# Kernel optimization log

Measured on AMD Instinct MI355X. Metric: run time of the kernel, lower is better.

Reference implementation:

```python
import jax, jax.numpy as jnp
import numpy as np

B = 1024          # batch
H = 512           # hidden_dim
T = 256           # seq_len
CD = 2            # coord_dim
LAT = 64 + 64 + 128  # total latent dim


def setup_inputs() -> dict:
    key = jax.random.key(0)
    ks = jax.random.split(key, 20)
    s = 0.05  # weight init scale
    rn = lambda k, shp: (jax.random.normal(k, shp, dtype=jnp.float32) * s)
    return {
        "z_primitive": jax.random.normal(ks[0], (B, 64), dtype=jnp.float32),
        "z_skill": jax.random.normal(ks[1], (B, 64), dtype=jnp.float32),
        "z_style": jax.random.normal(ks[2], (B, 128), dtype=jnp.float32),
        "W_proj": rn(ks[3], (2 * H, LAT)),
        "b_proj": jnp.zeros((2 * H,), jnp.float32),
        "Wih1": rn(ks[4], (4 * H, CD)),
        "Whh1": rn(ks[5], (4 * H, H)),
        "bih1": jnp.zeros((4 * H,), jnp.float32),
        "bhh1": jnp.zeros((4 * H,), jnp.float32),
        "Wih2": rn(ks[6], (4 * H, H)),
        "Whh2": rn(ks[7], (4 * H, H)),
        "bih2": jnp.zeros((4 * H,), jnp.float32),
        "bhh2": jnp.zeros((4 * H,), jnp.float32),
        "Wo1": rn(ks[8], (H // 2, H)),
        "bo1": jnp.zeros((H // 2,), jnp.float32),
        "Wo2": rn(ks[9], (CD, H // 2)),
        "bo2": jnp.zeros((CD,), jnp.float32),
    }


def _lstm_cell(x, h, c, Wih, Whh, bih, bhh):
    # PyTorch gate order: i, f, g, o
    gates = x @ Wih.T + h @ Whh.T + (bih + bhh)
    i, f, g, o = jnp.split(gates, 4, axis=1)
    c_new = jax.nn.sigmoid(f) * c + jax.nn.sigmoid(i) * jnp.tanh(g)
    h_new = jax.nn.sigmoid(o) * jnp.tanh(c_new)
    return h_new, c_new


def reference(z_primitive, z_skill, z_style, W_proj, b_proj,
              Wih1, Whh1, bih1, bhh1, Wih2, Whh2, bih2, bhh2,
              Wo1, bo1, Wo2, bo2):
    z = jnp.concatenate([z_primitive, z_skill, z_style], axis=1)  # [B, LAT]
    init = z @ W_proj.T + b_proj                                  # [B, 2H]
    h0 = init[:, :H]
    c0 = init[:, H:]
    x0 = jnp.zeros((z.shape[0], CD), init.dtype)

    def step(carry, _):
        x, h1, c1, h2, c2 = carry
        h1, c1 = _lstm_cell(x, h1, c1, Wih1, Whh1, bih1, bhh1)
        h2, c2 = _lstm_cell(h1, h2, c2, Wih2, Whh2, bih2, bhh2)
        # output MLP (Dropout inactive in eval)
        y = jax.nn.relu(h2 @ Wo1.T + bo1) @ Wo2.T + bo2  # [B, CD]
        return (y, h1, c1, h2, c2), y

    # h0/c0 repeated across both LSTM layers (repeat(2,1,1) in torch)
    _, ys = jax.lax.scan(step, (x0, h0, c0, h0, c0), None, length=T)
    return jnp.transpose(ys, (1, 0, 2))  # [B, T, CD]
```

## Files before the change

kernel.cpp:

```cpp
#include <hip/hip_runtime.h>
#include <math.h>

#define NB 1024
#define NH 512
#define NT 256
#define NCD 2

typedef unsigned short u16;
typedef __bf16 bf16x8 __attribute__((ext_vector_type(8)));
typedef float  f32x4  __attribute__((ext_vector_type(4)));
typedef unsigned int  u32x4 __attribute__((ext_vector_type(4)));

#define MFMA_BF16 __builtin_amdgcn_mfma_f32_16x16x32_bf16

__device__ __forceinline__ float sigf(float x) { return 1.0f / (1.0f + expf(-x)); }
__device__ __forceinline__ u16 f2b(float f) {
    union { float f; unsigned i; } v; v.f = f;
    unsigned r = v.i + 0x7fffu + ((v.i >> 16) & 1u);
    return (u16)(r >> 16);
}

__device__ __forceinline__ void async_cp16(const void* gptr, void* lptr) {
    __builtin_amdgcn_global_load_lds(
        (const __attribute__((address_space(1))) unsigned int*)gptr,
        (__attribute__((address_space(3))) unsigned int*)lptr,
        16, 0, 0);
}

__device__ __forceinline__ u32x4 aload16(const u16* p) {
    unsigned* q = (unsigned*)(void*)p;
    u32x4 v;
    v.x = __hip_atomic_load(q + 0, __ATOMIC_RELAXED, __HIP_MEMORY_SCOPE_AGENT);
    v.y = __hip_atomic_load(q + 1, __ATOMIC_RELAXED, __HIP_MEMORY_SCOPE_AGENT);
    v.z = __hip_atomic_load(q + 2, __ATOMIC_RELAXED, __HIP_MEMORY_SCOPE_AGENT);
    v.w = __hip_atomic_load(q + 3, __ATOMIC_RELAXED, __HIP_MEMORY_SCOPE_AGENT);
    return v;
}

__global__ __launch_bounds__(256) void convert3(
    const float* __restrict__ a, const float* __restrict__ b,
    const float* __restrict__ c,
    u16* __restrict__ oa, u16* __restrict__ ob, u16* __restrict__ oc)
{
    const int i = blockIdx.x * 256 + threadIdx.x;
    oa[i] = f2b(a[i]); ob[i] = f2b(b[i]); oc[i] = f2b(c[i]);
}

__global__ __launch_bounds__(256) void convw1(
    const float* __restrict__ a, u16* __restrict__ o)
{
    const int i = blockIdx.x * 256 + threadIdx.x;
    o[i] = f2b(a[i]);
}

__global__ __launch_bounds__(256) void bsum_k(
    const float* __restrict__ bi1, const float* __restrict__ bh1,
    const float* __restrict__ bi2, const float* __restrict__ bh2,
    float* __restrict__ o1, float* __restrict__ o2)
{
    const int i = blockIdx.x * 256 + threadIdx.x;
    o1[i] = bi1[i] + bh1[i];
    o2[i] = bi2[i] + bh2[i];
}

__global__ __launch_bounds__(512) void zero_bar(unsigned* __restrict__ b)
{
    b[threadIdx.x] = 0u;
}

__global__ __launch_bounds__(256) void init_kernel(
    const float* __restrict__ zp, const float* __restrict__ zs,
    const float* __restrict__ zst, const float* __restrict__ Wp,
    const float* __restrict__ bp,
    u16* __restrict__ h1, float* __restrict__ c1,
    u16* __restrict__ h2, float* __restrict__ c2)
{
    __shared__ float z[4][256];
    const int tid = threadIdx.x;
    const int b0  = blockIdx.x * 4;
    for (int i = tid; i < 4 * 256; i += 256) {
        const int bb = i >> 8, k = i & 255;
        float v;
        if (k < 64)       v = zp [(b0 + bb) * 64  + k];
        else if (k < 128) v = zs [(b0 + bb) * 64  + (k - 64)];
        else              v = zst[(b0 + bb) * 128 + (k - 128)];
        z[bb][k] = v;
    }
    __syncthreads();
    for (int rt = 0; rt < 4; ++rt) {
        const int r = rt * 256 + tid;
        const float bias = bp[r];
        float a0 = bias, a1 = bias, a2 = bias, a3 = bias;
        for (int k = 0; k < 256; ++k) {
            const float w = Wp[r * 256 + k];
            a0 += z[0][k] * w; a1 += z[1][k] * w;
            a2 += z[2][k] * w; a3 += z[3][k] * w;
        }
        const float acc[4] = {a0, a1, a2, a3};
        for (int bb = 0; bb < 4; ++bb) {
            const int b = b0 + bb;
            if (r < NH) {
                h1[b * NH + r] = f2b(acc[bb]);
                h2[b * NH + r] = f2b(acc[bb]);
            } else {
                c1[b * NH + r - NH] = acc[bb];
                c2[b * NH + r - NH] = acc[bb];
            }
        }
    }
}

__global__ __launch_bounds__(512, 4) void step_fused(
    const u16* __restrict__ h2prev,
    const u16* __restrict__ A0,
    const u16* __restrict__ W0,
    const float* __restrict__ bsum1,
    const float* __restrict__ Wx,
    const u16* __restrict__ W1b,
    const float* __restrict__ bo1, const float* __restrict__ Wo2,
    const float* __restrict__ bo2, float* __restrict__ outp,
    float* __restrict__ c1, u16* __restrict__ h1next,
    const u16* __restrict__ Wih2b, const u16* __restrict__ Whh2b,
    const float* __restrict__ bsum2,
    float* __restrict__ c2, const u16* __restrict__ h2cur,
    u16* __restrict__ h2next,
    unsigned* bar,
    const int t, const int do_lstm)
{
    __shared__ __align__(16) char smem[61440];
    float* eg  = (float*)smem;
    float* red = (float*)(smem + 36864);

    const int tid  = threadIdx.x;
    const int lane = tid & 63;
    const int wv   = tid >> 6;
    const int g    = wv & 3;
    const int mh   = wv >> 2;
    const int l15  = lane & 15;
    const int q    = lane >> 4;
    const int bx   = blockIdx.x;
    const int ut   = (bx & 7) * 2 + ((bx >> 3) & 1);
    const int grp  = bx >> 4;
    const int b0   = grp * 32;
    const int u0   = ut * 32;

    int goffW0, goffW1, goffA = 0, goffO[4];
    {
        const int c0 = (wv * 2) * 64 + lane;
        const int w0r = c0 >> 3;
        goffW0 = ((w0r >> 5) * NH + u0 + (w0r & 31)) * NH + (((c0 & 7) ^ (w0r & 7)) * 8);
        const int c1i = (wv * 2 + 1) * 64 + lane;
        const int w1r = c1i >> 3;
        goffW1 = ((w1r >> 5) * NH + u0 + (w1r & 31)) * NH + (((c1i & 7) ^ (w1r & 7)) * 8);
        if (wv < 4) {
            const int ca = wv * 64 + lane;
            const int ar = ca >> 3;
            goffA = (b0 + ar) * NH + (((ca & 7) ^ (ar & 7)) * 8);
        }
#pragma unroll
        for (int i = 0; i < 4; ++i) {
            const int cidx = (wv * 4 + i) * 64 + lane;
            const int row  = cidx >> 3;
            const int kc   = (cidx & 7) ^ (row & 7);
            goffO[i] = row * NH + kc * 8;
        }
    }

    auto issue = [&](int m, int bi) {
        const int k0 = (m & 7) * 64;
        char* base = smem + bi * 20480;
        async_cp16((const void*)(W0 + goffW0 + k0),
                   (void*)(base + 4096 + (wv * 2) * 1024));
        async_cp16((const void*)(W0 + goffW1 + k0),
                   (void*)(base + 4096 + (wv * 2 + 1) * 1024));
        if (wv < 4)
            async_cp16((const void*)(A0 + goffA + k0),
                       (void*)(base + wv * 1024));
    };
    auto issueW2 = [&](const u16* Wp, int m, int bi) {
        const int k0 = (m & 7) * 64;
        char* base = smem + bi * 20480;
        async_cp16((const void*)(Wp + goffW0 + k0), (void*)(base + 4096 + (wv * 2) * 1024));
        async_cp16((const void*)(Wp + goffW1 + k0), (void*)(base + 4096 + (wv * 2 + 1) * 1024));
    };
    auto awrite = [&](char* base, u32x4 v) {
        *(u32x4*)(base + wv * 1024 + lane * 16) = v;
    };

    const int u_e  = tid & 31;
    const int bq_e = tid >> 5;
    const int ug_e = u0 + u_e;
    float bs1r[4], bs2r[4], wx0[4], wx1[4], c1pre[2], c2pre[2];
#pragma unroll
    for (int g4 = 0; g4 < 4; ++g4) {
        bs1r[g4] = bsum1[g4 * NH + ug_e];
        bs2r[g4] = bsum2[g4 * NH + ug_e];
        wx0[g4]  = Wx[(g4 * NH + ug_e) * 2 + 0];
        wx1[g4]  = Wx[(g4 * NH + ug_e) * 2 + 1];
    }
    c1pre[0] = c1[(size_t)(b0 + bq_e * 2 + 0) * NH + ug_e];
    c1pre[1] = c1[(size_t)(b0 + bq_e * 2 + 1) * NH + ug_e];
    c2pre[0] = c2[(size_t)(b0 + bq_e * 2 + 0) * NH + ug_e];
    c2pre[1] = c2[(size_t)(b0 + bq_e * 2 + 1) * NH + ug_e];

    if (do_lstm) issue(0, 2);

    float r_x[4] = {0.f, 0.f, 0.f, 0.f};

    if (h2prev) {
        f32x4 acc_o[2][2];
#pragma unroll
        for (int mi = 0; mi < 2; ++mi)
#pragma unroll
            for (int ni = 0; ni < 2; ++ni)
                acc_o[mi][ni] = (f32x4){0.f, 0.f, 0.f, 0.f};

        for (int kk = 0; kk < 8; ++kk) {
            __syncthreads();
            const int k0 = kk * 64;
#pragma unroll
            for (int i = 0; i < 4; ++i)
                async_cp16((const void*)(W1b + goffO[i] + k0),
                           (void*)(smem + ((wv * 4 + i) << 10)));
            if (wv < 4)
                async_cp16((const void*)(h2prev + goffA + k0),
                           (void*)(smem + 32768 + (wv << 10)));
            asm volatile("s_waitcnt vmcnt(0)" ::: "memory");
            __builtin_amdgcn_s_barrier();
#pragma unroll
            for (int kh = 0; kh < 2; ++kh) {
                bf16x8 bfr[2], av[2];
#pragma unroll
                for (int ni = 0; ni < 2; ++ni) {
                    const int wrow = wv * 32 + ni * 16 + l15;
                    const int j = (kh * 4 + q) ^ (wrow & 7);
                    bfr[ni] = *(const bf16x8*)(smem + wrow * 128 + j * 16);
                }
#pragma unroll
                for (int mi = 0; mi < 2; ++mi) {
                    const int row = mi * 16 + l15;
                    const int j = (kh * 4 + q) ^ (row & 7);
                    av[mi] = *(const bf16x8*)(smem + 32768 + row * 128 + j * 16);
                }
#pragma unroll
                for (int mi = 0; mi < 2; ++mi)
#pragma unroll
                    for (int ni = 0; ni < 2; ++ni)
                        acc_o[mi][ni] = MFMA_BF16(av[mi], bfr[ni], acc_o[mi][ni], 0, 0, 0);
            }
        }
        float bo1n[2], w20[2], w21[2];
#pragma unroll
        for (int ni = 0; ni < 2; ++ni) {
            const int n = wv * 32 + ni * 16 + l15;
            bo1n[ni] = bo1[n]; w20[ni] = Wo2[n]; w21[ni] = Wo2[256 + n];
        }
        float pa[2][4], pb[2][4];
#pragma unroll
        for (int mi = 0; mi < 2; ++mi)
#pragma unroll
            for (int r = 0; r < 4; ++r) {
                const float s0 = fmaxf(acc_o[mi][0][r] + bo1n[0], 0.f);
                const float s1 = fmaxf(acc_o[mi][1][r] + bo1n[1], 0.f);
                pa[mi][r] = s0 * w20[0] + s1 * w20[1];
                pb[mi][r] = s0 * w21[0] + s1 * w21[1];
            }
#pragma unroll
        for (int off = 1; off < 16; off <<= 1)
#pragma unroll
            for (int mi = 0; mi < 2; ++mi)
#pragma unroll
                for (int r = 0; r < 4; ++r) {
                    pa[mi][r] += __shfl_xor(pa[mi][r], off, 64);
                    pb[mi][r] += __shfl_xor(pb[mi][r], off, 64);
                }
        if (l15 == 0) {
#pragma unroll
            for (int mi = 0; mi < 2; ++mi)
#pragma unroll
                for (int r = 0; r < 4; ++r) {
                    const int m = mi * 16 + q * 4 + r;
                    red[m * 16 + wv * 2 + 0] = pa[mi][r];
                    red[m * 16 + wv * 2 + 1] = pb[mi][r];
                }
        }
        __syncthreads();
        if (ut == 0 && tid < 64) {
            const int bl = tid >> 1, cc = tid & 1;
            float y = bo2[cc];
#pragma unroll
            for (int w8 = 0; w8 < 8; ++w8) y += red[bl * 16 + w8 * 2 + cc];
            outp[(size_t)(b0 + bl) * (NT * NCD) + (t - 1) * NCD + cc] = y;
        }
        if (do_lstm) {
#pragma unroll
            for (int jj = 0; jj < 2; ++jj)
#pragma unroll
                for (int cc = 0; cc < 2; ++cc) {
                    float y = bo2[cc];
#pragma unroll
                    for (int w8 = 0; w8 < 8; ++w8)
                        y += red[(bq_e * 2 + jj) * 16 + w8 * 2 + cc];
                    r_x[jj * 2 + cc] = y;
                }
        }
        __syncthreads();
    }
    if (!do_lstm) return;

    {
        f32x4 acc[2];
        acc[0] = (f32x4){0.f, 0.f, 0.f, 0.f};
        acc[1] = (f32x4){0.f, 0.f, 0.f, 0.f};
        const int M = 8;
        issue(1, 0);
        int ci = 2;
        for (int m = 0; m < M; ++m) {
            if (m + 1 < M) {
                if (wv < 4) asm volatile("s_waitcnt vmcnt(3)" ::: "memory");
                else        asm volatile("s_waitcnt vmcnt(2)" ::: "memory");
            } else {
                asm volatile("s_waitcnt vmcnt(0)" ::: "memory");
            }
            __builtin_amdgcn_s_barrier();
            if (m + 2 < M) {
                int bi = ci + 2; if (bi >= 3) bi -= 3;
                issue(m + 2, bi);
            }
            const char* bA = smem + ci * 20480;
            const char* bW = bA + 4096;
#pragma unroll
            for (int khi = 0; khi < 2; ++khi) {
                bf16x8 bfr[2];
#pragma unroll
                for (int ni = 0; ni < 2; ++ni) {
                    const int wrow = g * 32 + ni * 16 + l15;
                    const int j = (khi * 4 + q) ^ (wrow & 7);
                    bfr[ni] = *(const bf16x8*)(bW + wrow * 128 + j * 16);
                }
                const int row = mh * 16 + l15;
                const int j = (khi * 4 + q) ^ (row & 7);
                const bf16x8 av = *(const bf16x8*)(bA + row * 128 + j * 16);
                acc[0] = MFMA_BF16(av, bfr[0], acc[0], 0, 0, 0);
                acc[1] = MFMA_BF16(av, bfr[1], acc[1], 0, 0, 0);
            }
            ++ci; if (ci == 3) ci = 0;
        }

        __syncthreads();
#pragma unroll
        for (int ni = 0; ni < 2; ++ni)
#pragma unroll
            for (int r = 0; r < 4; ++r)
                eg[(g * 32 + mh * 16 + q * 4 + r) * 33 + ni * 16 + l15] = acc[ni][r];
        __syncthreads();

#pragma unroll
        for (int jj = 0; jj < 2; ++jj) {
            const int bl = bq_e * 2 + jj;
            const int b  = b0 + bl;
            float gv[4];
#pragma unroll
            for (int g4 = 0; g4 < 4; ++g4) gv[g4] = eg[(g4 * 32 + bl) * 33 + u_e] + bs1r[g4];
            const float x0 = r_x[jj * 2 + 0];
            const float x1 = r_x[jj * 2 + 1];
#pragma unroll
            for (int g4 = 0; g4 < 4; ++g4) gv[g4] += x0 * wx0[g4] + x1 * wx1[g4];
            const float iv = sigf(gv[0]);
            const float fv = sigf(gv[1]);
            const float gg = tanhf(gv[2]);
            const float ov = sigf(gv[3]);
            const size_t idx = (size_t)b * NH + ug_e;
            const float cn = fv * c1pre[jj] + iv * gg;
            c1[idx] = cn;
            const unsigned hb = (unsigned)f2b(ov * tanhf(cn));
            const unsigned pr = (unsigned)__shfl_xor((int)hb, 1, 64);
            if (!(u_e & 1))
                __hip_atomic_store((unsigned*)(void*)(h1next + idx),
                                   hb | (pr << 16),
                                   __ATOMIC_RELAXED, __HIP_MEMORY_SCOPE_AGENT);
        }
    }

    {
        unsigned* mybar = bar + grp * 16;
        const unsigned target = 16u * (unsigned)(t + 1);
        __syncthreads();
        if (tid == 0) {
            __hip_atomic_fetch_add(mybar, 1u, __ATOMIC_RELAXED, __HIP_MEMORY_SCOPE_AGENT);
            int guard = 0;
            while (__hip_atomic_load(mybar, __ATOMIC_RELAXED, __HIP_MEMORY_SCOPE_AGENT)
                       < target && ++guard < (1 << 20)) {
                __builtin_amdgcn_s_sleep(1);
            }
        }
        __syncthreads();
    }

    {
        f32x4 acc[2];
        acc[0] = (f32x4){0.f, 0.f, 0.f, 0.f};
        acc[1] = (f32x4){0.f, 0.f, 0.f, 0.f};
        u32x4 rB0, rB1;
        if (wv < 4) rB0 = aload16(h1next + goffA);
        issueW2(Wih2b, 0, 0);
        if (wv < 4) rB1 = aload16(h1next + goffA + 64);
        issueW2(Wih2b, 1, 1);
        if (wv < 4) {
            awrite(smem + 0 * 20480, rB0);
            awrite(smem + 1 * 20480, rB1);
            rB0 = aload16(h1next + goffA + 128);
        }
        int ci = 0;
        for (int m = 0; m < 16; ++m) {
            if (m + 1 < 16) {
                if (wv < 4) asm volatile("s_waitcnt vmcnt(6) lgkmcnt(0)" ::: "memory");
                else        asm volatile("s_waitcnt vmcnt(2)" ::: "memory");
            } else {
                asm volatile("s_waitcnt vmcnt(0) lgkmcnt(0)" ::: "memory");
            }
            __builtin_amdgcn_s_barrier();
            if (m + 2 < 16) {
                int bi = ci + 2; if (bi >= 3) bi -= 3;
                if (wv < 4) awrite(smem + bi * 20480, (m & 1) ? rB1 : rB0);
                issueW2((m + 2 < 8) ? Wih2b : Whh2b, m + 2, bi);
                if (wv < 4 && m + 3 < 16) {
                    const u16* Ap = (m + 3 < 8) ? h1next : h2cur;
                    const int k0 = ((m + 3) & 7) * 64;
                    if (m & 1) rB0 = aload16(Ap + goffA + k0);
                    else       rB1 = aload16(Ap + goffA + k0);
                }
            }
            const char* bA = smem + ci * 20480;
            const char* bW = bA + 4096;
#pragma unroll
            for (int khi = 0; khi < 2; ++khi) {
                bf16x8 bfr[2];
#pragma unroll
                for (int ni = 0; ni < 2; ++ni) {
                    const int wrow = g * 32 + ni * 16 + l15;
                    const int j = (khi * 4 + q) ^ (wrow & 7);
                    bfr[ni] = *(const bf16x8*)(bW + wrow * 128 + j * 16);
                }
                const int row = mh * 16 + l15;
                const int j = (khi * 4 + q) ^ (row & 7);
                const bf16x8 av = *(const bf16x8*)(bA + row * 128 + j * 16);
                acc[0] = MFMA_BF16(av, bfr[0], acc[0], 0, 0, 0);
                acc[1] = MFMA_BF16(av, bfr[1], acc[1], 0, 0, 0);
            }
            ++ci; if (ci == 3) ci = 0;
        }

        __syncthreads();
#pragma unroll
        for (int ni = 0; ni < 2; ++ni)
#pragma unroll
            for (int r = 0; r < 4; ++r)
                eg[(g * 32 + mh * 16 + q * 4 + r) * 33 + ni * 16 + l15] = acc[ni][r];
        __syncthreads();

#pragma unroll
        for (int jj = 0; jj < 2; ++jj) {
            const int bl = bq_e * 2 + jj;
            const int b  = b0 + bl;
            float gv[4];
#pragma unroll
            for (int g4 = 0; g4 < 4; ++g4) gv[g4] = eg[(g4 * 32 + bl) * 33 + u_e] + bs2r[g4];
            const float iv = sigf(gv[0]);
            const float fv = sigf(gv[1]);
            const float gg = tanhf(gv[2]);
            const float ov = sigf(gv[3]);
            const size_t idx = (size_t)b * NH + ug_e;
            const float cn = fv * c2pre[jj] + iv * gg;
            c2[idx] = cn;
            h2next[idx] = f2b(ov * tanhf(cn));
        }
    }
}

extern "C" void kernel_launch(void* const* d_in, const int* in_sizes, int n_in,
                              void* d_out, int out_size, void* d_ws, size_t ws_size,
                              hipStream_t stream)
{
    const float* zp   = (const float*)d_in[0];
    const float* zsk  = (const float*)d_in[1];
    const float* zst  = (const float*)d_in[2];
    const float* Wp   = (const float*)d_in[3];
    const float* bp   = (const float*)d_in[4];
    const float* Wih1 = (const float*)d_in[5];
    const float* Whh1 = (const float*)d_in[6];
    const float* bih1 = (const float*)d_in[7];
    const float* bhh1 = (const float*)d_in[8];
    const float* Wih2 = (const float*)d_in[9];
    const float* Whh2 = (const float*)d_in[10];
    const float* bih2 = (const float*)d_in[11];
    const float* bhh2 = (const float*)d_in[12];
    const float* Wo1  = (const float*)d_in[13];
    const float* bo1  = (const float*)d_in[14];
    const float* Wo2  = (const float*)d_in[15];
    const float* bo2  = (const float*)d_in[16];

    const size_t BH = (size_t)NB * NH;
    u16*   h1a   = (u16*)d_ws;
    u16*   h1b   = h1a + BH;
    u16*   h2a   = h1b + BH;
    u16*   h2b   = h2a + BH;
    float* c1    = (float*)(h2b + BH);
    float* c2    = c1 + BH;
    float* bs1   = c2 + BH;
    float* bs2   = bs1 + 2048;
    u16*   Wo1b  = (u16*)(bs2 + 2048);
    u16*   Whh1b = Wo1b + 131072;
    u16*   Wih2b = Whh1b + 1048576;
    u16*   Whh2b = Wih2b + 1048576;
    unsigned* bar = (unsigned*)(Whh2b + 1048576);

    convert3<<<(2048 * 512) / 256, 256, 0, stream>>>(Whh1, Wih2, Whh2, Whh1b, Wih2b, Whh2b);
    convw1<<<(256 * 512) / 256, 256, 0, stream>>>(Wo1, Wo1b);
    bsum_k<<<2048 / 256, 256, 0, stream>>>(bih1, bhh1, bih2, bhh2, bs1, bs2);
    init_kernel<<<NB / 4, 256, 0, stream>>>(zp, zsk, zst, Wp, bp, h1a, c1, h2a, c2);
    zero_bar<<<1, 512, 0, stream>>>(bar);

    u16* h1c = h1a; u16* h1n = h1b;
    u16* h2c = h2a; u16* h2n = h2b;
    float* outp = (float*)d_out;
    for (int t = 0; t < NT; ++t) {
        step_fused<<<512, 512, 0, stream>>>(
            (t == 0) ? (const u16*)0 : h2c, h1c, Whh1b, bs1, Wih1,
            Wo1b, bo1, Wo2, bo2, outp, c1, h1n,
            Wih2b, Whh2b, bs2, c2, h2c, h2n, bar, t, 1);
        u16* tmp = h1c; h1c = h1n; h1n = tmp;
        tmp = h2c; h2c = h2n; h2n = tmp;
    }
    step_fused<<<512, 512, 0, stream>>>(
        h2c, h1c, Whh1b, bs1, Wih1,
        Wo1b, bo1, Wo2, bo2, outp, c1, h1n,
        Wih2b, Whh2b, bs2, c2, h2c, h2n, bar, NT, 0);
}
```

Before: 8.335 ms.

## Split output MLP across blocks with atomic reduction and reorder layer-2 GEMM to overlap barrier

Each block now computes only its 16-column slice of the output MLP, with a triple-buffered async-copy pipeline. Partial results are accumulated into the output with atomicAdd, so the output is zeroed beforehand. A per-group barrier makes all blocks' partial sums visible before the next input x is read back. Layer 2 now runs the h2·Whh2 half first and waits on a second barrier for h1next only partway through, overlapping that barrier with useful MFMA work. The cost is extra atomics and grid-level barrier traffic, and correctness depends on relaxed-atomic visibility and the barrier counter layout.

```diff
diff --git a/kernel.cpp b/kernel.cpp
--- a/kernel.cpp
+++ b/kernel.cpp
@@ -25,6 +25,10 @@
         (const __attribute__((address_space(1))) unsigned int*)gptr,
         (__attribute__((address_space(3))) unsigned int*)lptr,
         16, 0, 0);
+}
+
+__device__ __forceinline__ float aloadf(const float* p) {
+    return __hip_atomic_load((float*)p, __ATOMIC_RELAXED, __HIP_MEMORY_SCOPE_AGENT);
 }
 
 __device__ __forceinline__ u32x4 aload16(const u16* p) {
@@ -66,6 +70,11 @@
 __global__ __launch_bounds__(512) void zero_bar(unsigned* __restrict__ b)
 {
     b[threadIdx.x] = 0u;
+}
+
+__global__ __launch_bounds__(512) void zero_out(float* __restrict__ o)
+{
+    o[blockIdx.x * 512 + threadIdx.x] = 0.f;
 }
 
 __global__ __launch_bounds__(256) void init_kernel(
@@ -111,7 +120,7 @@
 }
 
 __global__ __launch_bounds__(512, 4) void step_fused(
-    const u16* __restrict__ h2prev,
+    const u16* __restrict__ h2c,
     const u16* __restrict__ A0,
     const u16* __restrict__ W0,
     const float* __restrict__ bsum1,
@@ -122,14 +131,12 @@
     float* __restrict__ c1, u16* __restrict__ h1next,
     const u16* __restrict__ Wih2b, const u16* __restrict__ Whh2b,
     const float* __restrict__ bsum2,
-    float* __restrict__ c2, const u16* __restrict__ h2cur,
-    u16* __restrict__ h2next,
-    unsigned* bar,
+    float* __restrict__ c2, u16* __restrict__ h2next,
+    unsigned* __restrict__ bar,
     const int t, const int do_lstm)
 {
     __shared__ __align__(16) char smem[61440];
     float* eg  = (float*)smem;
-    float* red = (float*)(smem + 36864);
 
     const int tid  = threadIdx.x;
     const int lane = tid & 63;
@@ -143,8 +150,9 @@
     const int grp  = bx >> 4;
     const int b0   = grp * 32;
     const int u0   = ut * 32;
-
-    int goffW0, goffW1, goffA = 0, goffO[4];
+    const bool has_prev = (t > 0);
+
+    int goffW0, goffW1, goffA = 0, goffWS = 0;
     {
         const int c0 = (wv * 2) * 64 + lane;
         const int w0r = c0 >> 3;
@@ -157,12 +165,10 @@
             const int ar = ca >> 3;
             goffA = (b0 + ar) * NH + (((ca & 7) ^ (ar & 7)) * 8);
         }
-#pragma unroll
-        for (int i = 0; i < 4; ++i) {
-            const int cidx = (wv * 4 + i) * 64 + lane;
-            const int row  = cidx >> 3;
-            const int kc   = (cidx & 7) ^ (row & 7);
-            goffO[i] = row * NH + kc * 8;
+        if (wv == 4 || wv == 5) {
+            const int cs = (wv - 4) * 64 + lane;
+            const int rl = cs >> 3;
+            goffWS = (ut * 16 + rl) * NH + (((cs & 7) ^ (rl & 7)) * 8);
         }
     }
 
@@ -205,65 +211,59 @@
 
     if (do_lstm) issue(0, 2);
 
-    float r_x[4] = {0.f, 0.f, 0.f, 0.f};
-
-    if (h2prev) {
-        f32x4 acc_o[2][2];
+    if (has_prev) {
+        f32x4 acc_o[2];
+        acc_o[0] = (f32x4){0.f, 0.f, 0.f, 0.f};
+        acc_o[1] = (f32x4){0.f, 0.f, 0.f, 0.f};
+
+        auto issue_pa = [&](int k, int pb) {
+            const int k0 = k * 64;
+            char* base = smem + pb * 8192;
+            if (wv < 4)
+                async_cp16((const void*)(h2c + goffA + k0),
+                           (void*)(base + (wv << 10)));
+            if (wv == 4 || wv == 5)
+                async_cp16((const void*)(W1b + goffWS + k0),
+                           (void*)(base + 4096 + ((wv - 4) << 10)));
+        };
+        issue_pa(0, 0);
+        issue_pa(1, 1);
+        int cp = 0;
+        for (int kk = 0; kk < 8; ++kk) {
+            if (kk + 1 < 8)
+                asm volatile("s_waitcnt vmcnt(1)" ::: "memory");
+            else
+                asm volatile("s_waitcnt vmcnt(0)" ::: "memory");
+            __builtin_amdgcn_s_barrier();
+            if (kk + 2 < 8) {
+                int pb = cp + 2; if (pb >= 3) pb -= 3;
+                issue_pa(kk + 2, pb);
+            }
+            const char* pbase = smem + cp * 8192;
+#pragma unroll
+            for (int kh = 0; kh < 2; ++kh) {
+                const int j = (kh * 4 + q) ^ (l15 & 7);
+                const bf16x8 bfr = *(const bf16x8*)(pbase + 4096 + l15 * 128 + j * 16);
+#pragma unroll
+                for (int mi = 0; mi < 2; ++mi) {
+                    const bf16x8 av = *(const bf16x8*)(pbase + (mi * 16 + l15) * 128 + j * 16);
+                    acc_o[mi] = MFMA_BF16(av, bfr, acc_o[mi], 0, 0, 0);
+                }
+            }
+            ++cp; if (cp == 3) cp = 0;
+        }
+        const int ng = ut * 16 + l15;
+        const float bo1n = bo1[ng];
+        const float w20  = Wo2[ng];
+        const float w21  = Wo2[256 + ng];
+        float pa[2][4], pb[2][4];
 #pragma unroll
         for (int mi = 0; mi < 2; ++mi)
 #pragma unroll
-            for (int ni = 0; ni < 2; ++ni)
-                acc_o[mi][ni] = (f32x4){0.f, 0.f, 0.f, 0.f};
-
-        for (int kk = 0; kk < 8; ++kk) {
-            __syncthreads();
-            const int k0 = kk * 64;
-#pragma unroll
-            for (int i = 0; i < 4; ++i)
-                async_cp16((const void*)(W1b + goffO[i] + k0),
-                           (void*)(smem + ((wv * 4 + i) << 10)));
-            if (wv < 4)
-                async_cp16((const void*)(h2prev + goffA + k0),
-                           (void*)(smem + 32768 + (wv << 10)));
-            asm volatile("s_waitcnt vmcnt(0)" ::: "memory");
-            __builtin_amdgcn_s_barrier();
-#pragma unroll
-            for (int kh = 0; kh < 2; ++kh) {
-                bf16x8 bfr[2], av[2];
-#pragma unroll
-                for (int ni = 0; ni < 2; ++ni) {
-                    const int wrow = wv * 32 + ni * 16 + l15;
-                    const int j = (kh * 4 + q) ^ (wrow & 7);
-                    bfr[ni] = *(const bf16x8*)(smem + wrow * 128 + j * 16);
-                }
-#pragma unroll
-                for (int mi = 0; mi < 2; ++mi) {
-                    const int row = mi * 16 + l15;
-                    const int j = (kh * 4 + q) ^ (row & 7);
-                    av[mi] = *(const bf16x8*)(smem + 32768 + row * 128 + j * 16);
-                }
-#pragma unroll
-                for (int mi = 0; mi < 2; ++mi)
-#pragma unroll
-                    for (int ni = 0; ni < 2; ++ni)
-                        acc_o[mi][ni] = MFMA_BF16(av[mi], bfr[ni], acc_o[mi][ni], 0, 0, 0);
-            }
-        }
-        float bo1n[2], w20[2], w21[2];
-#pragma unroll
-        for (int ni = 0; ni < 2; ++ni) {
-            const int n = wv * 32 + ni * 16 + l15;
-            bo1n[ni] = bo1[n]; w20[ni] = Wo2[n]; w21[ni] = Wo2[256 + n];
-        }
-        float pa[2][4], pb[2][4];
-#pragma unroll
-        for (int mi = 0; mi < 2; ++mi)
-#pragma unroll
             for (int r = 0; r < 4; ++r) {
-                const float s0 = fmaxf(acc_o[mi][0][r] + bo1n[0], 0.f);
-                const float s1 = fmaxf(acc_o[mi][1][r] + bo1n[1], 0.f);
-                pa[mi][r] = s0 * w20[0] + s1 * w20[1];
-                pb[mi][r] = s0 * w21[0] + s1 * w21[1];
+                const float s = fmaxf(acc_o[mi][r] + bo1n, 0.f);
+                pa[mi][r] = s * w20;
+                pb[mi][r] = s * w21;
             }
 #pragma unroll
         for (int off = 1; off < 16; off <<= 1)
@@ -274,44 +274,27 @@
                     pa[mi][r] += __shfl_xor(pa[mi][r], off, 64);
                     pb[mi][r] += __shfl_xor(pb[mi][r], off, 64);
                 }
-        if (l15 == 0) {
+        if (wv == 0 && l15 == 0) {
+            const float b20 = (ut == 0) ? bo2[0] : 0.f;
+            const float b21 = (ut == 0) ? bo2[1] : 0.f;
 #pragma unroll
             for (int mi = 0; mi < 2; ++mi)
 #pragma unroll
                 for (int r = 0; r < 4; ++r) {
                     const int m = mi * 16 + q * 4 + r;
-                    red[m * 16 + wv * 2 + 0] = pa[mi][r];
-                    red[m * 16 + wv * 2 + 1] = pb[mi][r];
+                    float* dst = outp + (size_t)(b0 + m) * (NT * NCD) + (t - 1) * NCD;
+                    atomicAdd(dst + 0, pa[mi][r] + b20);
+                    atomicAdd(dst + 1, pb[mi][r] + b21);
                 }
         }
         __syncthreads();
-        if (ut == 0 && tid < 64) {
-            const int bl = tid >> 1, cc = tid & 1;
-            float y = bo2[cc];
-#pragma unroll
-            for (int w8 = 0; w8 < 8; ++w8) y += red[bl * 16 + w8 * 2 + cc];
-            outp[(size_t)(b0 + bl) * (NT * NCD) + (t - 1) * NCD + cc] = y;
-        }
-        if (do_lstm) {
-#pragma unroll
-            for (int jj = 0; jj < 2; ++jj)
-#pragma unroll
-                for (int cc = 0; cc < 2; ++cc) {
-                    float y = bo2[cc];
-#pragma unroll
-                    for (int w8 = 0; w8 < 8; ++w8)
-                        y += red[(bq_e * 2 + jj) * 16 + w8 * 2 + cc];
-                    r_x[jj * 2 + cc] = y;
-                }
-        }
-        __syncthreads();
     }
     if (!do_lstm) return;
 
+    f32x4 acc[2];
+    acc[0] = (f32x4){0.f, 0.f, 0.f, 0.f};
+    acc[1] = (f32x4){0.f, 0.f, 0.f, 0.f};
     {
-        f32x4 acc[2];
-        acc[0] = (f32x4){0.f, 0.f, 0.f, 0.f};
-        acc[1] = (f32x4){0.f, 0.f, 0.f, 0.f};
         const int M = 8;
         issue(1, 0);
         int ci = 2;
@@ -346,70 +329,84 @@
             }
             ++ci; if (ci == 3) ci = 0;
         }
-
-        __syncthreads();
-#pragma unroll
-        for (int ni = 0; ni < 2; ++ni)
-#pragma unroll
-            for (int r = 0; r < 4; ++r)
-                eg[(g * 32 + mh * 16 + q * 4 + r) * 33 + ni * 16 + l15] = acc[ni][r];
-        __syncthreads();
-
-#pragma unroll
-        for (int jj = 0; jj < 2; ++jj) {
-            const int bl = bq_e * 2 + jj;
-            const int b  = b0 + bl;
-            float gv[4];
-#pragma unroll
-            for (int g4 = 0; g4 < 4; ++g4) gv[g4] = eg[(g4 * 32 + bl) * 33 + u_e] + bs1r[g4];
-            const float x0 = r_x[jj * 2 + 0];
-            const float x1 = r_x[jj * 2 + 1];
-#pragma unroll
-            for (int g4 = 0; g4 < 4; ++g4) gv[g4] += x0 * wx0[g4] + x1 * wx1[g4];
-            const float iv = sigf(gv[0]);
-            const float fv = sigf(gv[1]);
-            const float gg = tanhf(gv[2]);
-            const float ov = sigf(gv[3]);
-            const size_t idx = (size_t)b * NH + ug_e;
-            const float cn = fv * c1pre[jj] + iv * gg;
-            c1[idx] = cn;
-            const unsigned hb = (unsigned)f2b(ov * tanhf(cn));
-            const unsigned pr = (unsigned)__shfl_xor((int)hb, 1, 64);
-            if (!(u_e & 1))
-                __hip_atomic_store((unsigned*)(void*)(h1next + idx),
-                                   hb | (pr << 16),
-                                   __ATOMIC_RELAXED, __HIP_MEMORY_SCOPE_AGENT);
-        }
-    }
-
-    {
-        unsigned* mybar = bar + grp * 16;
-        const unsigned target = 16u * (unsigned)(t + 1);
+    }
+
+    float r_x[4] = {0.f, 0.f, 0.f, 0.f};
+    if (has_prev) {
+        unsigned* mybar0 = bar + grp * 16;
+        const unsigned target = 16u * (unsigned)t;
         __syncthreads();
         if (tid == 0) {
-            __hip_atomic_fetch_add(mybar, 1u, __ATOMIC_RELAXED, __HIP_MEMORY_SCOPE_AGENT);
+            __hip_atomic_fetch_add(mybar0, 1u, __ATOMIC_RELAXED, __HIP_MEMORY_SCOPE_AGENT);
             int guard = 0;
-            while (__hip_atomic_load(mybar, __ATOMIC_RELAXED, __HIP_MEMORY_SCOPE_AGENT)
+            while (__hip_atomic_load(mybar0, __ATOMIC_RELAXED, __HIP_MEMORY_SCOPE_AGENT)
                        < target && ++guard < (1 << 20)) {
                 __builtin_amdgcn_s_sleep(1);
             }
         }
         __syncthreads();
-    }
+#pragma unroll
+        for (int jj = 0; jj < 2; ++jj) {
+            const float* src = outp + (size_t)(b0 + bq_e * 2 + jj) * (NT * NCD)
+                               + (t - 1) * NCD;
+            r_x[jj * 2 + 0] = aloadf(src + 0);
+            r_x[jj * 2 + 1] = aloadf(src + 1);
+        }
+    }
+
+    __syncthreads();
+#pragma unroll
+    for (int ni = 0; ni < 2; ++ni)
+#pragma unroll
+        for (int r = 0; r < 4; ++r)
+            eg[(g * 32 + mh * 16 + q * 4 + r) * 33 + ni * 16 + l15] = acc[ni][r];
+    __syncthreads();
+
+#pragma unroll
+    for (int jj = 0; jj < 2; ++jj) {
+        const int bl = bq_e * 2 + jj;
+        const int b  = b0 + bl;
+        float gv[4];
+#pragma unroll
+        for (int g4 = 0; g4 < 4; ++g4) gv[g4] = eg[(g4 * 32 + bl) * 33 + u_e] + bs1r[g4];
+        const float x0 = r_x[jj * 2 + 0];
+        const float x1 = r_x[jj * 2 + 1];
+#pragma unroll
+        for (int g4 = 0; g4 < 4; ++g4) gv[g4] += x0 * wx0[g4] + x1 * wx1[g4];
+        const float iv = sigf(gv[0]);
+        const float fv = sigf(gv[1]);
+        const float gg = tanhf(gv[2]);
+        const float ov = sigf(gv[3]);
+        const size_t idx = (size_t)b * NH + ug_e;
+        const float cn = fv * c1pre[jj] + iv * gg;
+        c1[idx] = cn;
+        const unsigned hb = (unsigned)f2b(ov * tanhf(cn));
+        const unsigned pr = (unsigned)__shfl_xor((int)hb, 1, 64);
+        if (!(u_e & 1))
+            __hip_atomic_store((unsigned*)(void*)(h1next + idx),
+                               hb | (pr << 16),
+                               __ATOMIC_RELAXED, __HIP_MEMORY_SCOPE_AGENT);
+    }
+
+    unsigned* mybar1 = bar + grp * 16 + 8;
+    const unsigned target1 = 16u * (unsigned)(t + 1);
+    __syncthreads();
+    if (tid == 0)
+        __hip_atomic_fetch_add(mybar1, 1u, __ATOMIC_RELAXED, __HIP_MEMORY_SCOPE_AGENT);
 
     {
-        f32x4 acc[2];
-        acc[0] = (f32x4){0.f, 0.f, 0.f, 0.f};
-        acc[1] = (f32x4){0.f, 0.f, 0.f, 0.f};
+        f32x4 acc2[2];
+        acc2[0] = (f32x4){0.f, 0.f, 0.f, 0.f};
+        acc2[1] = (f32x4){0.f, 0.f, 0.f, 0.f};
         u32x4 rB0, rB1;
-        if (wv < 4) rB0 = aload16(h1next + goffA);
-        issueW2(Wih2b, 0, 0);
-        if (wv < 4) rB1 = aload16(h1next + goffA + 64);
-        issueW2(Wih2b, 1, 1);
+        if (wv < 4) rB0 = aload16(h2c + goffA);
+        issueW2(Whh2b, 0, 0);
+        if (wv < 4) rB1 = aload16(h2c + goffA + 64);
+        issueW2(Whh2b, 1, 1);
         if (wv < 4) {
             awrite(smem + 0 * 20480, rB0);
             awrite(smem + 1 * 20480, rB1);
-            rB0 = aload16(h1next + goffA + 128);
+            rB0 = aload16(h2c + goffA + 128);
         }
         int ci = 0;
         for (int m = 0; m < 16; ++m) {
@@ -420,12 +417,22 @@
                 asm volatile("s_waitcnt vmcnt(0) lgkmcnt(0)" ::: "memory");
             }
             __builtin_amdgcn_s_barrier();
+            if (m == 4) {
+                if (tid == 0) {
+                    int guard = 0;
+                    while (__hip_atomic_load(mybar1, __ATOMIC_RELAXED, __HIP_MEMORY_SCOPE_AGENT)
+                               < target1 && ++guard < (1 << 20)) {
+                        __builtin_amdgcn_s_sleep(1);
+                    }
+                }
+                __syncthreads();
+            }
             if (m + 2 < 16) {
                 int bi = ci + 2; if (bi >= 3) bi -= 3;
                 if (wv < 4) awrite(smem + bi * 20480, (m & 1) ? rB1 : rB0);
-                issueW2((m + 2 < 8) ? Wih2b : Whh2b, m + 2, bi);
+                issueW2((m + 2 < 8) ? Whh2b : Wih2b, m + 2, bi);
                 if (wv < 4 && m + 3 < 16) {
-                    const u16* Ap = (m + 3 < 8) ? h1next : h2cur;
+                    const u16* Ap = (m + 3 < 8) ? h2c : h1next;
                     const int k0 = ((m + 3) & 7) * 64;
                     if (m & 1) rB0 = aload16(Ap + goffA + k0);
                     else       rB1 = aload16(Ap + goffA + k0);
@@ -445,8 +452,8 @@
                 const int row = mh * 16 + l15;
                 const int j = (khi * 4 + q) ^ (row & 7);
                 const bf16x8 av = *(const bf16x8*)(bA + row * 128 + j * 16);
-                acc[0] = MFMA_BF16(av, bfr[0], acc[0], 0, 0, 0);
-                acc[1] = MFMA_BF16(av, bfr[1], acc[1], 0, 0, 0);
+                acc2[0] = MFMA_BF16(av, bfr[0], acc2[0], 0, 0, 0);
+                acc2[1] = MFMA_BF16(av, bfr[1], acc2[1], 0, 0, 0);
             }
             ++ci; if (ci == 3) ci = 0;
         }
@@ -456,7 +463,7 @@
         for (int ni = 0; ni < 2; ++ni)
 #pragma unroll
             for (int r = 0; r < 4; ++r)
-                eg[(g * 32 + mh * 16 + q * 4 + r) * 33 + ni * 16 + l15] = acc[ni][r];
+                eg[(g * 32 + mh * 16 + q * 4 + r) * 33 + ni * 16 + l15] = acc2[ni][r];
         __syncthreads();
 
 #pragma unroll
@@ -520,20 +527,21 @@
     bsum_k<<<2048 / 256, 256, 0, stream>>>(bih1, bhh1, bih2, bhh2, bs1, bs2);
     init_kernel<<<NB / 4, 256, 0, stream>>>(zp, zsk, zst, Wp, bp, h1a, c1, h2a, c2);
     zero_bar<<<1, 512, 0, stream>>>(bar);
+    zero_out<<<(NB * NT * NCD) / 512, 512, 0, stream>>>((float*)d_out);
 
     u16* h1c = h1a; u16* h1n = h1b;
     u16* h2c = h2a; u16* h2n = h2b;
     float* outp = (float*)d_out;
     for (int t = 0; t < NT; ++t) {
         step_fused<<<512, 512, 0, stream>>>(
-            (t == 0) ? (const u16*)0 : h2c, h1c, Whh1b, bs1, Wih1,
+            h2c, h1c, Whh1b, bs1, Wih1,
             Wo1b, bo1, Wo2, bo2, outp, c1, h1n,
-            Wih2b, Whh2b, bs2, c2, h2c, h2n, bar, t, 1);
+            Wih2b, Whh2b, bs2, c2, h2n, bar, t, 1);
         u16* tmp = h1c; h1c = h1n; h1n = tmp;
         tmp = h2c; h2c = h2n; h2n = tmp;
     }
     step_fused<<<512, 512, 0, stream>>>(
         h2c, h1c, Whh1b, bs1, Wih1,
         Wo1b, bo1, Wo2, bo2, outp, c1, h1n,
-        Wih2b, Whh2b, bs2, c2, h2c, h2n, bar, NT, 0);
-}
+        Wih2b, Whh2b, bs2, c2, h2n, bar, NT, 0);
+}
```

Result: no change. 8.467 ms (+1.6%).
